# Kernel tuning notes

Measured on AMD Instinct MI355X. Metric: run time of the kernel, lower is better.

The kernel has to match this reference:

```python
import jax, jax.numpy as jnp
import numpy as np

N_NODES = 50000
N_EDGES = 1000000
IN_CH = 128
OUT_CH = 128
N_HEADS = 8
CIS = 8.0


def _edge_conv(x, e, wq, bq, wk, bk, wv, bv, n_heads, cis):
    """One EdgeConv layer (PyG mean aggregation, source_to_target flow)."""
    src, dst = e[0], e[1]                       # x_j = x[src], x_i = x[dst]
    xi = x[dst]
    xj = x[src]
    feat = jnp.concatenate([xi, xj - xi], axis=1)        # [E, 2C]
    q = feat @ wq + bq                                   # [E, O]
    k = feat @ wk + bk
    v = feat @ wv + bv
    E, O = q.shape
    hs = O // n_heads
    q = q.reshape(E, n_heads, hs)
    k = k.reshape(E, n_heads, hs)
    v = v.reshape(E, n_heads, hs)
    # edge_weight = sign(log|dst-src| - log(cis))
    d = jnp.abs(dst - src).astype(q.dtype)
    ew = jnp.sign(jnp.log(d) - jnp.log(jnp.asarray(cis, q.dtype)))
    v = v * ew[:, None, None]
    scale = jnp.asarray(1.0 / np.sqrt(hs), q.dtype)
    probs = jax.nn.softmax(q * k * scale, axis=-1)       # softmax over head_size
    ctx = (probs * v).reshape(E, O)                      # [E, O]
    n = x.shape[0]
    s = jax.ops.segment_sum(ctx, dst, num_segments=n)    # mean aggr over targets
    cnt = jax.ops.segment_sum(jnp.ones((E,), ctx.dtype), dst, num_segments=n)
    return s / jnp.maximum(cnt, 1.0)[:, None]


def setup_inputs() -> dict:
    key = jax.random.key(0)
    ks = jax.random.split(key, 24)
    x = jax.random.normal(ks[0], (N_NODES, IN_CH), jnp.float32)
    edge_index = jax.random.randint(ks[1], (2, N_EDGES), 0, N_NODES, dtype=jnp.int32)
    half = N_EDGES // 2
    e0 = edge_index[:, jax.random.permutation(ks[2], N_EDGES)[:half]]
    e1 = edge_index[:, jax.random.permutation(ks[3], N_EDGES)[:half]]
    e2 = edge_index[:, jax.random.permutation(ks[4], N_EDGES)[:half]]
    batch = jnp.zeros((N_NODES,), jnp.int32)

    def mk(k, i, o):
        return jax.random.normal(k, (i, o), jnp.float32) * 0.02

    def mkb(k, o):
        return jax.random.normal(k, (o,), jnp.float32) * 0.02

    # layer dims: conv0 128->128, conv1 128->64, conv2 64->128
    return dict(
        x=x, e0=e0, e1=e1, e2=e2, batch=batch,
        wq0=mk(ks[5], 2 * IN_CH, OUT_CH), bq0=mkb(ks[6], OUT_CH),
        wk0=mk(ks[7], 2 * IN_CH, OUT_CH), bk0=mkb(ks[8], OUT_CH),
        wv0=mk(ks[9], 2 * IN_CH, OUT_CH), bv0=mkb(ks[10], OUT_CH),
        wq1=mk(ks[11], 2 * OUT_CH, OUT_CH // 2), bq1=mkb(ks[12], OUT_CH // 2),
        wk1=mk(ks[13], 2 * OUT_CH, OUT_CH // 2), bk1=mkb(ks[14], OUT_CH // 2),
        wv1=mk(ks[15], 2 * OUT_CH, OUT_CH // 2), bv1=mkb(ks[16], OUT_CH // 2),
        wq2=mk(ks[17], OUT_CH, OUT_CH), bq2=mkb(ks[18], OUT_CH),
        wk2=mk(ks[19], OUT_CH, OUT_CH), bk2=mkb(ks[20], OUT_CH),
        wv2=mk(ks[21], OUT_CH, OUT_CH), bv2=mkb(ks[22], OUT_CH),
    )


def reference(x, e0, e1, e2, batch,
              wq0, bq0, wk0, bk0, wv0, bv0,
              wq1, bq1, wk1, bk1, wv1, bv1,
              wq2, bq2, wk2, bk2, wv2, bv2):
    x0 = jax.nn.relu(_edge_conv(x, e0, wq0, bq0, wk0, bk0, wv0, bv0, N_HEADS, CIS))
    h = jax.nn.relu(_edge_conv(x0, e1, wq1, bq1, wk1, bk1, wv1, bv1, N_HEADS, CIS))
    h = _edge_conv(h, e2, wq2, bq2, wk2, bk2, wv2, bv2, N_HEADS, CIS)
    return jax.nn.relu(h + x0)
```

## Files before the change

### kernel.cpp

```cpp
#include <hip/hip_runtime.h>
#include <hip/hip_fp16.h>


typedef _Float16 f16x8 __attribute__((ext_vector_type(8)));
typedef unsigned int u32x4 __attribute__((ext_vector_type(4)));
typedef float f32x4 __attribute__((ext_vector_type(4)));
typedef float f32x2 __attribute__((ext_vector_type(2)));

__device__ __forceinline__ unsigned short f2bf(float f) {
  unsigned int u = __float_as_uint(f);
  u += 0x7FFFu + ((u >> 16) & 1u);
  return (unsigned short)(u >> 16);
}
__device__ __forceinline__ unsigned short f2h(float f) {
  __half h = __float2half(f);
  return *reinterpret_cast<unsigned short*>(&h);
}
__device__ __forceinline__ __half2 ash2(unsigned w) {
  return *reinterpret_cast<__half2*>(&w);
}

__device__ __forceinline__ void pack_w_seg(const float* __restrict__ wq,
                                           const float* __restrict__ wk,
                                           const float* __restrict__ wv,
                                           unsigned short* __restrict__ dst,
                                           int IN, int O, float kscale, int id) {
  int kchunks = IN >> 5, nchunks = O >> 4;
  int total = 6 * nchunks * kchunks * 64;
  if (id >= total) return;
  int lane = id & 63;
  int frag = id >> 6;
  int kc = frag % kchunks;
  int nc = (frag / kchunks) % nchunks;
  int mat = frag / (kchunks * nchunks);
  const float* w = (mat % 3 == 0) ? wq : (mat % 3 == 1) ? wk : wv;
  float mul = (mat % 3 == 1) ? kscale : 1.0f;
  int n = nc * 16 + (lane & 15);
  int k0 = kc * 32 + (lane >> 4) * 8;
  unsigned short tmp[8];
#pragma unroll
  for (int j = 0; j < 8; ++j) {
    int row = k0 + j;
    float bot = w[(size_t)(IN + row) * O + n];
    float val = (mat < 3) ? (w[(size_t)row * O + n] - bot) : bot;
    tmp[j] = f2h(val * mul);
  }
  uint4 o;
  o.x = (unsigned)tmp[0] | ((unsigned)tmp[1] << 16);
  o.y = (unsigned)tmp[2] | ((unsigned)tmp[3] << 16);
  o.z = (unsigned)tmp[4] | ((unsigned)tmp[5] << 16);
  o.w = (unsigned)tmp[6] | ((unsigned)tmp[7] << 16);
  reinterpret_cast<uint4*>(dst)[id] = o;
}

__device__ __forceinline__ void pack_b_seg(const float* __restrict__ bq,
                                           const float* __restrict__ bk,
                                           const float* __restrict__ bv, float kscale, int O,
                                           float* __restrict__ out, int i) {
  int mat = i / O, c = i % O;
  float v = 0.f;
  if (mat == 0) v = bq[c];
  else if (mat == 1) v = bk[c] * kscale;
  else if (mat == 2) v = bv[c];
  out[i] = v;
}

__global__ void preproc(
    uint4* __restrict__ z0, int n0, uint4* __restrict__ z1, int n1,
    uint4* __restrict__ z2, int n2,
    const float* __restrict__ x, unsigned short* __restrict__ xb, int n8,
    const float* __restrict__ wq0, const float* __restrict__ wk0, const float* __restrict__ wv0,
    const float* __restrict__ wq1, const float* __restrict__ wk1, const float* __restrict__ wv1,
    const float* __restrict__ wq2, const float* __restrict__ wk2, const float* __restrict__ wv2,
    unsigned short* __restrict__ wp0, unsigned short* __restrict__ wp1,
    unsigned short* __restrict__ wp2,
    const float* __restrict__ bq0, const float* __restrict__ bk0, const float* __restrict__ bv0,
    const float* __restrict__ bq1, const float* __restrict__ bk1, const float* __restrict__ bv1,
    const float* __restrict__ bq2, const float* __restrict__ bk2, const float* __restrict__ bv2,
    float* __restrict__ bias0, float* __restrict__ bias1, float* __restrict__ bias2,
    float sc16, float sc8) {
  const int tid = blockIdx.x * blockDim.x + threadIdx.x;
  const int stride = gridDim.x * blockDim.x;
  const uint4 Z = make_uint4(0u, 0u, 0u, 0u);
  for (int j = tid; j < n0; j += stride) z0[j] = Z;
  for (int j = tid; j < n1; j += stride) z1[j] = Z;
  for (int j = tid; j < n2; j += stride) z2[j] = Z;
  for (int j = tid; j < n8; j += stride) {
    float4 a = reinterpret_cast<const float4*>(x)[2 * j];
    float4 b = reinterpret_cast<const float4*>(x)[2 * j + 1];
    uint4 o;
    o.x = (unsigned)f2h(a.x) | ((unsigned)f2h(a.y) << 16);
    o.y = (unsigned)f2h(a.z) | ((unsigned)f2h(a.w) << 16);
    o.z = (unsigned)f2h(b.x) | ((unsigned)f2h(b.y) << 16);
    o.w = (unsigned)f2h(b.z) | ((unsigned)f2h(b.w) << 16);
    reinterpret_cast<uint4*>(xb)[j] = o;
  }
  if (tid < 12288) pack_w_seg(wq0, wk0, wv0, wp0, 128, 128, sc16, tid);
  else if (tid < 18432) pack_w_seg(wq1, wk1, wv1, wp1, 128, 64, sc8, tid - 12288);
  else if (tid < 24576) pack_w_seg(wq2, wk2, wv2, wp2, 64, 128, sc16, tid - 18432);
  else if (tid < 24576 + 1920) {
    int i = tid - 24576;
    if (i < 768) pack_b_seg(bq0, bk0, bv0, sc16, 128, bias0, i);
    else if (i < 1152) pack_b_seg(bq1, bk1, bv1, sc8, 64, bias1, i - 768);
    else pack_b_seg(bq2, bk2, bv2, sc16, 128, bias2, i - 1152);
  }
}

__global__ void hist3(const int* __restrict__ e0, const int* __restrict__ e1,
                      const int* __restrict__ e2, int E, int* __restrict__ hist,
                      int* __restrict__ rank, int NP) {
  int i = blockIdx.x * blockDim.x + threadIdx.x;
  if (i >= E) return;
  rank[0 * E + i] = atomicAdd(&hist[0 * NP + e0[E + i]], 1);
  rank[1 * E + i] = atomicAdd(&hist[1 * NP + e1[E + i]], 1);
  rank[2 * E + i] = atomicAdd(&hist[2 * NP + e2[E + i]], 1);
}

__device__ __forceinline__ int block_scan_excl256(int v, int* buf, int t, int* total) {
  buf[t] = v;
  __syncthreads();
#pragma unroll
  for (int off = 1; off < 256; off <<= 1) {
    int add = (t >= off) ? buf[t - off] : 0;
    __syncthreads();
    buf[t] += add;
    __syncthreads();
  }
  int incl = buf[t];
  *total = buf[255];
  __syncthreads();
  return incl - v;
}

__global__ void scan_pass1(const int* __restrict__ hist, int* __restrict__ excl,
                           int* __restrict__ bsum, int n, int NP) {
  __shared__ int buf[256];
  int y = blockIdx.y, t = threadIdx.x;
  int i = blockIdx.x * 256 + t;
  int v = (i < n) ? hist[y * NP + i] : 0;
  int total;
  int ex = block_scan_excl256(v, buf, t, &total);
  if (i < NP) excl[y * NP + i] = ex;
  if (t == 0) bsum[y * 256 + blockIdx.x] = total;
}

__global__ void scan_pass2(int* __restrict__ bsum, int nblk) {
  __shared__ int buf[256];
  int y = blockIdx.y, t = threadIdx.x;
  int v = (t < nblk) ? bsum[y * 256 + t] : 0;
  int total;
  int ex = block_scan_excl256(v, buf, t, &total);
  bsum[y * 256 + t] = ex;
}

__global__ void scan_pass3(const int* __restrict__ excl, const int* __restrict__ bsum,
                           int* __restrict__ rowptr, int n, int NP, int RP, int E) {
  int y = blockIdx.y;
  int i = blockIdx.x * 256 + threadIdx.x;
  if (i < n) rowptr[y * RP + i] = excl[y * NP + i] + bsum[y * 256 + blockIdx.x];
  if (i == 0) rowptr[y * RP + n] = E;
}

__global__ void scatter3(const int* __restrict__ e0, const int* __restrict__ e1,
                         const int* __restrict__ e2, int E, const int* __restrict__ rowptr,
                         const int* __restrict__ rank, long long* __restrict__ pairs,
                         int NP, int RP) {
  int y = blockIdx.y;
  const int* e = (y == 0) ? e0 : (y == 1) ? e1 : e2;
  int i = blockIdx.x * 256 + threadIdx.x;
  if (i >= E) return;
  int sN = e[i], d = e[E + i];
  int pos = rowptr[y * RP + d] + rank[(size_t)y * E + i];
  long long val = ((long long)(unsigned)d << 32) | (unsigned)sN;
  __builtin_nontemporal_store(val, &pairs[(size_t)y * E + pos]);
}

template <int IN, int O, int G>
__global__ __launch_bounds__(256, 4) void node_gemm(
    const unsigned short* __restrict__ xb, int N, int NT,
    const unsigned short* __restrict__ wpack, const float* __restrict__ bias6,
    unsigned short* __restrict__ Y1, unsigned short* __restrict__ Y2) {
  constexpr int KC = IN / 32;
  constexpr int NCH = O / 16;
  constexpr int CHR = IN / 8;
  constexpr int CM = CHR - 1;
  __shared__ unsigned short tiles[64 * IN];

  const int chunk = gridDim.x >> 3;
  const int lb = (blockIdx.x & 7) * chunk + (blockIdx.x >> 3);
  if (lb >= NT * G) return;
  const int tile = lb / G;
  const int grp = lb % G;

  const int t = threadIdx.x, w = t >> 6, ln = t & 63;
  const int n0 = tile * 64;

  {
    constexpr int RPI = 64 / CHR;
    constexpr int NI = 16 / RPI;
    const int r_in = ln / CHR, c = ln % CHR;
#pragma unroll
    for (int i = 0; i < NI; ++i) {
      int row = w * 16 + i * RPI + r_in;
      int node = min(n0 + row, N - 1);
      int sc = c ^ (row & CM);
      const unsigned short* g = xb + (size_t)node * IN + sc * 8;
      unsigned short* l = &tiles[(size_t)(w * 16 + i * RPI) * IN];
      __builtin_amdgcn_global_load_lds(
          (const __attribute__((address_space(1))) unsigned int*)g,
          (__attribute__((address_space(3))) unsigned int*)l, 16, 0, 0);
    }
  }
  __syncthreads();

  const int col = ln & 15, quad = ln >> 4;
  const int g0 = grp * 8 + w * 2;

  f32x4 acc[2][4];
#pragma unroll
  for (int cc = 0; cc < 2; ++cc)
#pragma unroll
    for (int m = 0; m < 4; ++m) acc[cc][m] = (f32x4){0.f, 0.f, 0.f, 0.f};

#pragma unroll
  for (int kc = 0; kc < KC; ++kc) {
    f16x8 a[4];
#pragma unroll
    for (int m = 0; m < 4; ++m) {
      int row = m * 16 + col;
      int sc = (kc * 4 + quad) ^ (row & CM);
      a[m] = *reinterpret_cast<const f16x8*>(&tiles[(size_t)row * IN + sc * 8]);
    }
#pragma unroll
    for (int cc = 0; cc < 2; ++cc) {
      const f16x8 b = *reinterpret_cast<const f16x8*>(
          wpack + ((size_t)((g0 + cc) * KC + kc) * 64 + ln) * 8);
#pragma unroll
      for (int m = 0; m < 4; ++m)
        acc[cc][m] = __builtin_amdgcn_mfma_f32_16x16x32_f16(a[m], b, acc[cc][m], 0, 0, 0);
    }
  }

#pragma unroll
  for (int cc = 0; cc < 2; ++cc) {
    int gch = g0 + cc;
    int mat = gch / NCH, ncg = gch % NCH;
    unsigned short* Yp = (mat < 3) ? Y1 : Y2;
    int mo = (mat < 3) ? mat : mat - 3;
    float bv = bias6[gch * 16 + col];
    size_t coloff = (size_t)mo * O + ncg * 16 + col;
#pragma unroll
    for (int m = 0; m < 4; ++m)
#pragma unroll
      for (int r = 0; r < 4; ++r) {
        int node = n0 + m * 16 + quad * 4 + r;
        if (node < N) Yp[(size_t)node * (3 * O) + coloff] = f2h(acc[cc][m][r] + bv);
      }
  }
}

template <int O, int HS>
__global__ __launch_bounds__(512, 6) void edge_attn_kernel(
    const unsigned short* __restrict__ Y1, const unsigned short* __restrict__ Y2,
    const int2* __restrict__ pairs, const int E, float* __restrict__ s) {
  constexpr int NL = HS / 8;
  constexpr int PM = O / 4 - 1;
  __shared__ float ctx[64 * O];
  __shared__ int dstL[64];

  const int chunkB = gridDim.x >> 3;
  const int lb = (blockIdx.x & 7) * chunkB + (blockIdx.x >> 3);
  if (lb * 64 >= E) return;

  const int t = threadIdx.x;
  const int e = t >> 3, head = t & 7;
  const int eG = lb * 64 + e;
  const int eC = min(eG, E - 1);
  const bool valid = eG < E;
  const int2 p = pairs[eC];
  const int sN = p.x, dN = p.y;
  if ((t & 7) == 0) dstL[e] = dN;
  const float dd = fabsf((float)(dN - sN));
  const float ew = (dd > 8.f) ? 1.f : ((dd == 8.f) ? 0.f : -1.f);

  const unsigned short* b1 = Y1 + (size_t)dN * (3 * O) + head * HS;
  const unsigned short* b2 = Y2 + (size_t)sN * (3 * O) + head * HS;

  u32x4 q1[NL], q2[NL], k1[NL], k2[NL], v1[NL], v2[NL];
#pragma unroll
  for (int l = 0; l < NL; ++l) {
    q1[l] = *reinterpret_cast<const u32x4*>(b1 + l * 8);
    q2[l] = *reinterpret_cast<const u32x4*>(b2 + l * 8);
    k1[l] = *reinterpret_cast<const u32x4*>(b1 + O + l * 8);
    k2[l] = *reinterpret_cast<const u32x4*>(b2 + O + l * 8);
    v1[l] = *reinterpret_cast<const u32x4*>(b1 + 2 * O + l * 8);
    v2[l] = *reinterpret_cast<const u32x4*>(b2 + 2 * O + l * 8);
  }

  f32x2 ex2[NL * 4];
  f32x2 sum2 = (f32x2){0.f, 0.f};
#pragma unroll
  for (int l = 0; l < NL; ++l)
#pragma unroll
    for (int d = 0; d < 4; ++d) {
      __half2 qh = __hadd2(ash2(q1[l][d]), ash2(q2[l][d]));
      __half2 kh = __hadd2(ash2(k1[l][d]), ash2(k2[l][d]));
      __half2 qk = __hmul2(qh, kh);
      f32x2 eo;
      eo.x = exp2f(__low2float(qk));
      eo.y = exp2f(__high2float(qk));
      ex2[l * 4 + d] = eo;
      sum2 += eo;
    }
  const float sum = sum2.x + sum2.y;
  const float rs = valid ? (ew / sum) : 0.f;
  const f32x2 rs2 = (f32x2){rs, rs};
#pragma unroll
  for (int l = 0; l < NL; ++l) {
#pragma unroll
    for (int g2 = 0; g2 < 2; ++g2) {
      __half2 va = __hadd2(ash2(v1[l][g2 * 2]), ash2(v2[l][g2 * 2]));
      __half2 vb = __hadd2(ash2(v1[l][g2 * 2 + 1]), ash2(v2[l][g2 * 2 + 1]));
      f32x2 vva = (f32x2){__low2float(va), __high2float(va)};
      f32x2 vvb = (f32x2){__low2float(vb), __high2float(vb)};
      f32x2 oa = ex2[l * 4 + g2 * 2] * rs2 * vva;
      f32x2 ob = ex2[l * 4 + g2 * 2 + 1] * rs2 * vvb;
      f32x4 o = (f32x4){oa.x, oa.y, ob.x, ob.y};
      int g = l * 2 + g2;
      int pch = (g * 8 + head + e) & PM;
      *reinterpret_cast<f32x4*>(&ctx[e * O + pch * 4]) = o;
    }
  }
  __syncthreads();

  {
    constexpr int GRP = 512 / O;
    constexpr int EPT = 64 / GRP;
    const int hs2 = t & 7;
    const int cs = (t >> 3) & (HS - 1);
    const int colA = hs2 * HS + cs;
    const int seg0 = (t / O) * EPT;
    const int inv = (cs >> 2) * 8 + hs2;
    const int js = cs & 3;
    float run = 0.f;
    int runstart = 0;
    int dcur = dstL[seg0];
#pragma unroll
    for (int i = 0; i < EPT; ++i) {
      int ee = seg0 + i;
      int pch = (inv + ee) & PM;
      run += ctx[ee * O + pch * 4 + js];
      int dnext = (i < EPT - 1) ? dstL[ee + 1] : -1;
      if (dnext != dcur) {
        float* addr = &s[(size_t)dcur * O + colA];
        if (runstart > 0 && i < EPT - 1) *addr = run;
        else atomicAdd(addr, run);
        run = 0.f;
        runstart = i + 1;
        dcur = dnext;
      }
    }
  }
}

__global__ void finalize_relu_f32h(float* __restrict__ s, const int* __restrict__ rowptr,
                                   unsigned short* __restrict__ xbo, int total4, int Odiv4) {
  int i = blockIdx.x * blockDim.x + threadIdx.x;
  if (i >= total4) return;
  int node = i / Odiv4;
  float c = fmaxf((float)(rowptr[node + 1] - rowptr[node]), 1.0f);
  float4 v = reinterpret_cast<float4*>(s)[i];
  v.x = fmaxf(v.x / c, 0.f);
  v.y = fmaxf(v.y / c, 0.f);
  v.z = fmaxf(v.z / c, 0.f);
  v.w = fmaxf(v.w / c, 0.f);
  reinterpret_cast<float4*>(s)[i] = v;
  ushort4 o = make_ushort4(f2h(v.x), f2h(v.y), f2h(v.z), f2h(v.w));
  reinterpret_cast<ushort4*>(xbo)[i] = o;
}

__global__ void finalize_relu_h(const float* __restrict__ s, const int* __restrict__ rowptr,
                                unsigned short* __restrict__ xbo, int total4, int Odiv4) {
  int i = blockIdx.x * blockDim.x + threadIdx.x;
  if (i >= total4) return;
  int node = i / Odiv4;
  float c = fmaxf((float)(rowptr[node + 1] - rowptr[node]), 1.0f);
  float4 v = reinterpret_cast<const float4*>(s)[i];
  ushort4 o = make_ushort4(f2h(fmaxf(v.x / c, 0.f)), f2h(fmaxf(v.y / c, 0.f)),
                           f2h(fmaxf(v.z / c, 0.f)), f2h(fmaxf(v.w / c, 0.f)));
  reinterpret_cast<ushort4*>(xbo)[i] = o;
}

__global__ void finalize_add_relu(float* __restrict__ out, const float* __restrict__ x0,
                                  const int* __restrict__ rowptr, int total4, int Odiv4) {
  int i = blockIdx.x * blockDim.x + threadIdx.x;
  if (i >= total4) return;
  int node = i / Odiv4;
  float c = fmaxf((float)(rowptr[node + 1] - rowptr[node]), 1.0f);
  float4 v = reinterpret_cast<float4*>(out)[i];
  float4 r = reinterpret_cast<const float4*>(x0)[i];
  v.x = fmaxf(v.x / c + r.x, 0.f);
  v.y = fmaxf(v.y / c + r.y, 0.f);
  v.z = fmaxf(v.z / c + r.z, 0.f);
  v.w = fmaxf(v.w / c + r.w, 0.f);
  reinterpret_cast<float4*>(out)[i] = v;
}

extern "C" void kernel_launch(void* const* d_in, const int* in_sizes, int n_in,
                              void* d_out, int out_size, void* d_ws, size_t ws_size,
                              hipStream_t stream) {
  const float* x = (const float*)d_in[0];
  const int* e0 = (const int*)d_in[1];
  const int* e1 = (const int*)d_in[2];
  const int* e2 = (const int*)d_in[3];
  const float* wq0 = (const float*)d_in[5];
  const float* bq0 = (const float*)d_in[6];
  const float* wk0 = (const float*)d_in[7];
  const float* bk0 = (const float*)d_in[8];
  const float* wv0 = (const float*)d_in[9];
  const float* bv0 = (const float*)d_in[10];
  const float* wq1 = (const float*)d_in[11];
  const float* bq1 = (const float*)d_in[12];
  const float* wk1 = (const float*)d_in[13];
  const float* bk1 = (const float*)d_in[14];
  const float* wv1 = (const float*)d_in[15];
  const float* bv1 = (const float*)d_in[16];
  const float* wq2 = (const float*)d_in[17];
  const float* bq2 = (const float*)d_in[18];
  const float* wk2 = (const float*)d_in[19];
  const float* bk2 = (const float*)d_in[20];
  const float* wv2 = (const float*)d_in[21];
  const float* bv2 = (const float*)d_in[22];

  const int N = in_sizes[0] / 128;
  const int E = in_sizes[1] / 2;
  const int NBLK = (N + 255) / 256;
  const int NP = NBLK * 256;
  const int RP = NP + 256;
  const float LOG2E = 1.4426950408889634f;
  const float SC16 = 0.25f * LOG2E;
  const float SC8 = 0.35355339059327373f * LOG2E;

  unsigned short* wp0 = (unsigned short*)d_ws;
  unsigned short* wp1 = wp0 + 98304;
  unsigned short* wp2 = wp1 + 49152;
  float* bias0 = (float*)(wp2 + 49152);
  float* bias1 = bias0 + 768;
  float* bias2 = bias1 + 384;
  unsigned short* xb = (unsigned short*)(bias2 + 768);
  unsigned short* Y1 = xb + (size_t)N * 128;
  unsigned short* Y2 = Y1 + (size_t)N * 384;
  float* s0 = (float*)(Y2 + (size_t)N * 384);
  float* s1 = s0 + (size_t)N * 128;
  int* hist = (int*)(s1 + (size_t)N * 64);
  int* excl = hist + 3 * (size_t)NP;
  int* bsum = excl + 3 * (size_t)NP;
  int* rowptr = bsum + 768;
  int* rank = rowptr + 3 * (size_t)RP;
  long long* pairs = (long long*)(rank + 3 * (size_t)E + 2);

  preproc<<<2048, 256, 0, stream>>>(
      (uint4*)hist, 3 * NP / 4, (uint4*)s0, N * 48, (uint4*)d_out, out_size / 4,
      x, xb, N * 16,
      wq0, wk0, wv0, wq1, wk1, wv1, wq2, wk2, wv2, wp0, wp1, wp2,
      bq0, bk0, bv0, bq1, bk1, bv1, bq2, bk2, bv2, bias0, bias1, bias2,
      SC16, SC8);

  const int EB256 = (E + 255) / 256;
  hist3<<<EB256, 256, 0, stream>>>(e0, e1, e2, E, hist, rank, NP);
  scan_pass1<<<dim3(NBLK, 3), 256, 0, stream>>>(hist, excl, bsum, N, NP);
  scan_pass2<<<dim3(1, 3), 256, 0, stream>>>(bsum, NBLK);
  scan_pass3<<<dim3(NBLK, 3), 256, 0, stream>>>(excl, bsum, rowptr, N, NP, RP, E);
  scatter3<<<dim3(EB256, 3), 256, 0, stream>>>(e0, e1, e2, E, rowptr, rank, pairs, NP, RP);

  const int NT = (N + 63) / 64;
  const int EBK = (E + 63) / 64;
  const int EGRID = 8 * ((EBK + 7) / 8);
  const int GG6 = 8 * ((NT * 6 + 7) / 8);
  const int GG3 = 8 * ((NT * 3 + 7) / 8);

  node_gemm<128, 128, 6><<<GG6, 256, 0, stream>>>(xb, N, NT, wp0, bias0, Y1, Y2);
  edge_attn_kernel<128, 16><<<EGRID, 512, 0, stream>>>(Y1, Y2, (const int2*)pairs, E, s0);
  finalize_relu_f32h<<<(N * 32 + 255) / 256, 256, 0, stream>>>(s0, rowptr, xb, N * 32, 32);
  node_gemm<128, 64, 3><<<GG3, 256, 0, stream>>>(xb, N, NT, wp1, bias1, Y1, Y2);
  edge_attn_kernel<64, 8><<<EGRID, 512, 0, stream>>>(Y1, Y2, (const int2*)(pairs + E), E, s1);
  finalize_relu_h<<<(N * 16 + 255) / 256, 256, 0, stream>>>(s1, rowptr + RP, xb, N * 16, 16);
  node_gemm<64, 128, 6><<<GG6, 256, 0, stream>>>(xb, N, NT, wp2, bias2, Y1, Y2);
  edge_attn_kernel<128, 16><<<EGRID, 512, 0, stream>>>(Y1, Y2, (const int2*)(pairs + 2 * (size_t)E),
                                                       E, (float*)d_out);
  finalize_add_relu<<<(N * 32 + 255) / 256, 256, 0, stream>>>((float*)d_out, s0, rowptr + 2 * RP,
                                                              N * 32, 32);
}
```

Measured before the change: 523.9 us.

## Fuse edge histogram into preproc and CSR scatter into first node GEMM

The per-destination histogram atomics move into the preproc kernel, and the hist buffer is now zeroed with a memset beforehand. The edge scatter that builds sorted (dst,src) pairs runs as extra blocks appended to the first node_gemm launch. This removes two kernel launches and lets the scatter overlap the layer-0 GEMM. In exchange the GEMM kernel gains more parameters and a branch, and the histogram atomics now share preproc with the other grid-stride work.

Measured after the change: 520.5 us. About the same (-0.7%).

```diff
diff --git a/kernel.cpp b/kernel.cpp
--- a/kernel.cpp
+++ b/kernel.cpp
@@ -7,11 +7,6 @@
 typedef float f32x4 __attribute__((ext_vector_type(4)));
 typedef float f32x2 __attribute__((ext_vector_type(2)));
 
-__device__ __forceinline__ unsigned short f2bf(float f) {
-  unsigned int u = __float_as_uint(f);
-  u += 0x7FFFu + ((u >> 16) & 1u);
-  return (unsigned short)(u >> 16);
-}
 __device__ __forceinline__ unsigned short f2h(float f) {
   __half h = __float2half(f);
   return *reinterpret_cast<unsigned short*>(&h);
@@ -66,8 +61,9 @@
 }
 
 __global__ void preproc(
-    uint4* __restrict__ z0, int n0, uint4* __restrict__ z1, int n1,
-    uint4* __restrict__ z2, int n2,
+    const int* __restrict__ e0, const int* __restrict__ e1, const int* __restrict__ e2,
+    int E, int* __restrict__ hist, int* __restrict__ rank, int NP,
+    uint4* __restrict__ za, int na, uint4* __restrict__ zb, int nb,
     const float* __restrict__ x, unsigned short* __restrict__ xb, int n8,
     const float* __restrict__ wq0, const float* __restrict__ wk0, const float* __restrict__ wv0,
     const float* __restrict__ wq1, const float* __restrict__ wk1, const float* __restrict__ wv1,
@@ -81,10 +77,16 @@
     float sc16, float sc8) {
   const int tid = blockIdx.x * blockDim.x + threadIdx.x;
   const int stride = gridDim.x * blockDim.x;
+
+  for (int i = tid; i < E; i += stride) {
+    rank[i] = atomicAdd(&hist[e0[E + i]], 1);
+    rank[(size_t)E + i] = atomicAdd(&hist[NP + e1[E + i]], 1);
+    rank[2 * (size_t)E + i] = atomicAdd(&hist[2 * NP + e2[E + i]], 1);
+  }
+
   const uint4 Z = make_uint4(0u, 0u, 0u, 0u);
-  for (int j = tid; j < n0; j += stride) z0[j] = Z;
-  for (int j = tid; j < n1; j += stride) z1[j] = Z;
-  for (int j = tid; j < n2; j += stride) z2[j] = Z;
+  for (int j = tid; j < na; j += stride) za[j] = Z;
+  for (int j = tid; j < nb; j += stride) zb[j] = Z;
   for (int j = tid; j < n8; j += stride) {
     float4 a = reinterpret_cast<const float4*>(x)[2 * j];
     float4 b = reinterpret_cast<const float4*>(x)[2 * j + 1];
@@ -104,16 +106,6 @@
     else if (i < 1152) pack_b_seg(bq1, bk1, bv1, sc8, 64, bias1, i - 768);
     else pack_b_seg(bq2, bk2, bv2, sc16, 128, bias2, i - 1152);
   }
-}
-
-__global__ void hist3(const int* __restrict__ e0, const int* __restrict__ e1,
-                      const int* __restrict__ e2, int E, int* __restrict__ hist,
-                      int* __restrict__ rank, int NP) {
-  int i = blockIdx.x * blockDim.x + threadIdx.x;
-  if (i >= E) return;
-  rank[0 * E + i] = atomicAdd(&hist[0 * NP + e0[E + i]], 1);
-  rank[1 * E + i] = atomicAdd(&hist[1 * NP + e1[E + i]], 1);
-  rank[2 * E + i] = atomicAdd(&hist[2 * NP + e2[E + i]], 1);
 }
 
 __device__ __forceinline__ int block_scan_excl256(int v, int* buf, int t, int* total) {
@@ -161,32 +153,39 @@
   if (i == 0) rowptr[y * RP + n] = E;
 }
 
-__global__ void scatter3(const int* __restrict__ e0, const int* __restrict__ e1,
-                         const int* __restrict__ e2, int E, const int* __restrict__ rowptr,
-                         const int* __restrict__ rank, long long* __restrict__ pairs,
-                         int NP, int RP) {
-  int y = blockIdx.y;
-  const int* e = (y == 0) ? e0 : (y == 1) ? e1 : e2;
-  int i = blockIdx.x * 256 + threadIdx.x;
-  if (i >= E) return;
-  int sN = e[i], d = e[E + i];
-  int pos = rowptr[y * RP + d] + rank[(size_t)y * E + i];
-  long long val = ((long long)(unsigned)d << 32) | (unsigned)sN;
-  __builtin_nontemporal_store(val, &pairs[(size_t)y * E + pos]);
-}
-
-template <int IN, int O, int G>
+template <int IN, int O, int G, bool FS>
 __global__ __launch_bounds__(256, 4) void node_gemm(
     const unsigned short* __restrict__ xb, int N, int NT,
     const unsigned short* __restrict__ wpack, const float* __restrict__ bias6,
-    unsigned short* __restrict__ Y1, unsigned short* __restrict__ Y2) {
+    unsigned short* __restrict__ Y1, unsigned short* __restrict__ Y2,
+    int gemmBlks,
+    const int* __restrict__ e0, const int* __restrict__ e1, const int* __restrict__ e2,
+    int E, const int* __restrict__ rowptr, const int* __restrict__ rank,
+    long long* __restrict__ pairs, int RP) {
   constexpr int KC = IN / 32;
   constexpr int NCH = O / 16;
   constexpr int CHR = IN / 8;
   constexpr int CM = CHR - 1;
   __shared__ unsigned short tiles[64 * IN];
 
-  const int chunk = gridDim.x >> 3;
+  if (FS) {
+    if (blockIdx.x >= (unsigned)gemmBlks) {
+      const int sidx = blockIdx.x - gemmBlks;
+      const int EB = (E + 255) >> 8;
+      const int y = sidx / EB;
+      const int i = (sidx - y * EB) * 256 + threadIdx.x;
+      if (i < E) {
+        const int* e = (y == 0) ? e0 : (y == 1) ? e1 : e2;
+        int sN = e[i], d = e[E + i];
+        int pos = rowptr[y * RP + d] + rank[(size_t)y * E + i];
+        long long val = ((long long)(unsigned)d << 32) | (unsigned)sN;
+        __builtin_nontemporal_store(val, &pairs[(size_t)y * E + pos]);
+      }
+      return;
+    }
+  }
+
+  const int chunk = gemmBlks >> 3;
   const int lb = (blockIdx.x & 7) * chunk + (blockIdx.x >> 3);
   if (lb >= NT * G) return;
   const int tile = lb / G;
@@ -459,33 +458,39 @@
   int* rank = rowptr + 3 * (size_t)RP;
   long long* pairs = (long long*)(rank + 3 * (size_t)E + 2);
 
+  hipMemsetAsync(hist, 0, 3 * (size_t)NP * sizeof(int), stream);
+
   preproc<<<2048, 256, 0, stream>>>(
-      (uint4*)hist, 3 * NP / 4, (uint4*)s0, N * 48, (uint4*)d_out, out_size / 4,
+      e0, e1, e2, E, hist, rank, NP,
+      (uint4*)s0, N * 48, (uint4*)d_out, out_size / 4,
       x, xb, N * 16,
       wq0, wk0, wv0, wq1, wk1, wv1, wq2, wk2, wv2, wp0, wp1, wp2,
       bq0, bk0, bv0, bq1, bk1, bv1, bq2, bk2, bv2, bias0, bias1, bias2,
       SC16, SC8);
 
-  const int EB256 = (E + 255) / 256;
-  hist3<<<EB256, 256, 0, stream>>>(e0, e1, e2, E, hist, rank, NP);
   scan_pass1<<<dim3(NBLK, 3), 256, 0, stream>>>(hist, excl, bsum, N, NP);
   scan_pass2<<<dim3(1, 3), 256, 0, stream>>>(bsum, NBLK);
   scan_pass3<<<dim3(NBLK, 3), 256, 0, stream>>>(excl, bsum, rowptr, N, NP, RP, E);
-  scatter3<<<dim3(EB256, 3), 256, 0, stream>>>(e0, e1, e2, E, rowptr, rank, pairs, NP, RP);
 
   const int NT = (N + 63) / 64;
   const int EBK = (E + 63) / 64;
   const int EGRID = 8 * ((EBK + 7) / 8);
   const int GG6 = 8 * ((NT * 6 + 7) / 8);
   const int GG3 = 8 * ((NT * 3 + 7) / 8);
-
-  node_gemm<128, 128, 6><<<GG6, 256, 0, stream>>>(xb, N, NT, wp0, bias0, Y1, Y2);
+  const int EB256 = (E + 255) / 256;
+
+  node_gemm<128, 128, 6, true><<<GG6 + 3 * EB256, 256, 0, stream>>>(
+      xb, N, NT, wp0, bias0, Y1, Y2, GG6, e0, e1, e2, E, rowptr, rank, pairs, RP);
   edge_attn_kernel<128, 16><<<EGRID, 512, 0, stream>>>(Y1, Y2, (const int2*)pairs, E, s0);
   finalize_relu_f32h<<<(N * 32 + 255) / 256, 256, 0, stream>>>(s0, rowptr, xb, N * 32, 32);
-  node_gemm<128, 64, 3><<<GG3, 256, 0, stream>>>(xb, N, NT, wp1, bias1, Y1, Y2);
+  node_gemm<128, 64, 3, false><<<GG3, 256, 0, stream>>>(
+      xb, N, NT, wp1, bias1, Y1, Y2, GG3, nullptr, nullptr, nullptr, 0, nullptr, nullptr,
+      nullptr, 0);
   edge_attn_kernel<64, 8><<<EGRID, 512, 0, stream>>>(Y1, Y2, (const int2*)(pairs + E), E, s1);
   finalize_relu_h<<<(N * 16 + 255) / 256, 256, 0, stream>>>(s1, rowptr + RP, xb, N * 16, 16);
-  node_gemm<64, 128, 6><<<GG6, 256, 0, stream>>>(xb, N, NT, wp2, bias2, Y1, Y2);
+  node_gemm<64, 128, 6, false><<<GG6, 256, 0, stream>>>(
+      xb, N, NT, wp2, bias2, Y1, Y2, GG6, nullptr, nullptr, nullptr, 0, nullptr, nullptr,
+      nullptr, 0);
   edge_attn_kernel<128, 16><<<EGRID, 512, 0, stream>>>(Y1, Y2, (const int2*)(pairs + 2 * (size_t)E),
                                                        E, (float*)d_out);
   finalize_add_relu<<<(N * 32 + 255) / 256, 256, 0, stream>>>((float*)d_out, s0, rowptr + 2 * RP,
```
